# Kernel tuning notes

Measured on AMD Instinct MI355X. Metric: run time of the kernel, lower is better.

## Reference

```python
import jax, jax.numpy as jnp
import numpy as np

K = 3          # spline order
NUM = 32       # grid intervals G
IN_DIM = 256
OUT_DIM = 512
BATCH = 2048


def _b_spline_basis(x, grid, k):
    """Cox-de-Boor recursion. x: (B, I); grid: (I, G+2k+1) -> (B, I, G+k)."""
    xg = x[:, :, None]                      # (B, I, 1)
    g = grid[None, :, :]                    # (1, I, G+2k+1)
    val = ((xg >= g[:, :, :-1]) & (xg < g[:, :, 1:])).astype(x.dtype)
    for p in range(1, k + 1):
        left = (xg - g[:, :, :-(p + 1)]) / (g[:, :, p:-1] - g[:, :, :-(p + 1)])
        right = (g[:, :, p + 1:] - xg) / (g[:, :, p + 1:] - g[:, :, 1:-p])
        val = left * val[:, :, :-1] + right * val[:, :, 1:]
    return val                               # (B, I, G+k)


def setup_inputs() -> dict:
    key = jax.random.key(0)
    k1, k2, k3 = jax.random.split(key, 3)
    x = jax.random.normal(k1, (BATCH, IN_DIM), dtype=jnp.float32)
    # uniform grid on [-1, 1], extended by k knots on each side (extend_grid)
    base = np.linspace(-1.0, 1.0, NUM + 1)
    h = 2.0 / NUM
    ext = np.concatenate([base[0] - h * np.arange(K, 0, -1), base,
                          base[-1] + h * np.arange(1, K + 1)]).astype(np.float32)
    grid = jnp.tile(jnp.asarray(ext)[None, :], (IN_DIM, 1))  # (I, G+2k+1)
    coef = 0.1 * jax.random.normal(k2, (IN_DIM, OUT_DIM, NUM + K), dtype=jnp.float32)
    scale_base = jax.random.normal(k3, (IN_DIM, OUT_DIM), dtype=jnp.float32) / np.sqrt(IN_DIM).astype(np.float32)
    scale_sp = jnp.ones((IN_DIM, OUT_DIM), dtype=jnp.float32) / np.sqrt(IN_DIM).astype(np.float32)
    mask = jnp.ones((IN_DIM, OUT_DIM), dtype=jnp.float32)
    return {"x": x, "grid": grid, "coef": coef,
            "scale_base": scale_base, "scale_sp": scale_sp, "mask": mask}


def reference(x, grid, coef, scale_base, scale_sp, mask):
    base = jax.nn.silu(x)                                   # b(x) residual, (B, I)
    bases = _b_spline_basis(x, grid, K)                     # (B, I, G+k)
    # coef2curve: einsum('ijk,jlk->ijl') in pykan -> (B, I, O)
    y = jnp.einsum('bik,iok->bio', bases, coef)
    y = scale_base[None, :, :] * base[:, :, None] + scale_sp[None, :, :] * y
    y = mask[None, :, :] * y
    return jnp.sum(y, axis=1)                               # (B, O)
```

## Files before the change

### kernel.cpp

```cpp
#include <hip/hip_runtime.h>
#include <math.h>

#define BATCH   2048
#define IN_DIM  256
#define OUT_DIM 512
#define NK      35
#define KS      48
#define BTILE   128
#define OTILE   128
#define ICHUNK  32
#define NSPLIT  8
#define COEFS_BYTES ((size_t)IN_DIM * OUT_DIM * KS * 2)
#define PART_ELEMS  ((size_t)BATCH * OUT_DIM)

__device__ __forceinline__ unsigned short f2bf(float x) {
    unsigned u = __float_as_uint(x);
    u += 0x7FFF + ((u >> 16) & 1);
    return (unsigned short)(u >> 16);
}
__device__ __forceinline__ float bf2f(unsigned short h) {
    return __uint_as_float(((unsigned)h) << 16);
}
__device__ __forceinline__ unsigned pack2(unsigned short a, unsigned short b) {
    return (unsigned)a | ((unsigned)b << 16);
}

typedef __bf16 bf16x8 __attribute__((ext_vector_type(8)));
typedef float  f32x16 __attribute__((ext_vector_type(16)));
typedef unsigned int u32;

__device__ __forceinline__ void gload_lds16(const void* g, void* l) {
    __builtin_amdgcn_global_load_lds((const __attribute__((address_space(1))) u32*)g,
                                     (__attribute__((address_space(3))) u32*)l, 16, 0, 0);
}

#define PR 32
__global__ __launch_bounds__(256) void kan_prep(
    const float* __restrict__ coef,
    const float* __restrict__ scale_base,
    const float* __restrict__ scale_sp,
    const float* __restrict__ mask,
    unsigned short* __restrict__ coefS)
{
    __shared__ float sc[PR * NK];
    __shared__ float sspm[PR], ssbm[PR];
    const int t    = threadIdx.x;
    const int row0 = blockIdx.x * PR;

    {
        const float4* csrc = (const float4*)(coef + (size_t)row0 * NK);
        float4* cdst = (float4*)sc;
        cdst[t] = csrc[t];
        if (t < 24) cdst[t + 256] = csrc[t + 256];
    }
    if (t < PR) {
        float m = mask[row0 + t];
        sspm[t] = scale_sp[row0 + t] * m;
        ssbm[t] = scale_base[row0 + t] * m;
    }
    __syncthreads();

    if (t < PR * 6) {
        int r = t / 6;
        int q = t - r * 6;
        float spm = sspm[r];
        const float* c = sc + r * NK;
        uint4 v = make_uint4(0u, 0u, 0u, 0u);
        if (q < 4) {
            const float* cq = c + q * 8;
            v.x = pack2(f2bf(cq[0] * spm), f2bf(cq[1] * spm));
            v.y = pack2(f2bf(cq[2] * spm), f2bf(cq[3] * spm));
            v.z = pack2(f2bf(cq[4] * spm), f2bf(cq[5] * spm));
            v.w = pack2(f2bf(cq[6] * spm), f2bf(cq[7] * spm));
        } else if (q == 4) {
            float sbm = ssbm[r];
            unsigned short hi = f2bf(sbm);
            unsigned short lo = f2bf(sbm - bf2f(hi));
            v.x = pack2(f2bf(c[32] * spm), f2bf(c[33] * spm));
            v.y = pack2(f2bf(c[34] * spm), 0);
            v.z = pack2(hi, hi);
            v.w = pack2(lo, 0);
        }
        ((uint4*)coefS)[(size_t)(row0 + r) * 6 + q] = v;
    }
}

__global__ __launch_bounds__(256, 2) void kan_mfma(
    const float* __restrict__ x,
    const unsigned short* __restrict__ coefS,
    float* __restrict__ part)
{
    __shared__ __align__(16) short sA[2 * BTILE * KS];
    __shared__ __align__(16) short sB[2 * OTILE * KS];

    const int t    = threadIdx.x;
    const int w    = t >> 6;
    const int lane = t & 63;
    const int l31  = lane & 31, lh = lane >> 5;
    const int wr   = w & 1;
    const int wc   = w >> 1;
    const int o0   = blockIdx.x * OTILE;
    const int b0   = blockIdx.y * BTILE;
    const int ic0  = blockIdx.z * ICHUNK;
    const bool bTh = (t >= 128);
    const int wbase = t & 64;

    {
        uint4 z = make_uint4(0, 0, 0, 0);
        #pragma unroll
        for (int u = 0; u < 6; ++u) {
            int idx = t + 256 * u;
            if (idx < (2 * BTILE * KS * 2) / 16) ((uint4*)sA)[idx] = z;
        }
    }

    f32x16 acc00 = {}, acc01 = {}, acc10 = {}, acc11 = {};

    float xreg = 0.0f;
    int ojb0 = 0, ojb1 = 0;

    auto stageA = [&](short* arow, float xv, int& ojbn) {
        arow[ojbn] = 0; arow[ojbn + 1] = 0; arow[ojbn + 2] = 0; arow[ojbn + 3] = 0;
        float xn = (xv + 1.1875f) * 16.0f;
        float jf = floorf(xn);
        int   j  = (int)jf;
        float u  = xn - jf;
        bool valid = (xn >= 0.0f) && (j <= 37);
        float u2 = u * u, u3 = u2 * u;
        float w0 = (1.0f / 6.0f) * (1.0f - 3.0f * u + 3.0f * u2 - u3);
        float w1 = (1.0f / 6.0f) * (3.0f * u3 - 6.0f * u2 + 4.0f);
        float w2 = (1.0f / 6.0f) * (-3.0f * u3 + 3.0f * u2 + 3.0f * u + 1.0f);
        float w3 = (1.0f / 6.0f) * u3;
        int jb = j - 3;
        if (valid) {
            if ((unsigned)jb       < 35u) arow[jb]     = f2bf(w0);
            if ((unsigned)(jb + 1) < 35u) arow[jb + 1] = f2bf(w1);
            if ((unsigned)(jb + 2) < 35u) arow[jb + 2] = f2bf(w2);
            if ((unsigned)(jb + 3) < 35u) arow[jb + 3] = f2bf(w3);
        }
        ojbn = min(max(jb, 0), 31);
        float sig = 1.0f / (1.0f + __expf(-xv));
        float s   = xv * sig;
        unsigned short shi = f2bf(s);
        unsigned short slo = f2bf(s - bf2f(shi));
        *(unsigned int*)(arow + 36) = pack2(shi, slo);
        arow[38] = shi;
    };

    auto issueB = [&](int i, int buf) {
        const char* gsrc = (const char*)(coefS + ((size_t)i * OUT_DIM + o0) * KS);
        #pragma unroll
        for (int q = 0; q < 6; ++q) {
            int slot = wbase + (t & 63) + 128 * q;
            gload_lds16(gsrc + slot * 16,
                        (void*)(sB + buf * (OTILE * KS) + (wbase + 128 * q) * 8));
        }
    };

    __syncthreads();

    if (!bTh) {
        float x0 = x[(size_t)(b0 + t) * IN_DIM + ic0];
        stageA(sA + t * KS, x0, ojb0);
        xreg = x[(size_t)(b0 + t) * IN_DIM + ic0 + 1];
    } else {
        issueB(ic0, 0);
    }
    __syncthreads();

    auto body = [&](int it, int cur, int nxt, int& ojbn) {
        if (bTh && it + 1 < ICHUNK) issueB(ic0 + it + 1, nxt);

        const short* Ab = sA + cur * (BTILE * KS) + (wr * 64 + l31) * KS + lh * 8;
        const short* Bb = sB + cur * (OTILE * KS) + (wc * 64 + l31) * KS + lh * 8;
        #pragma unroll
        for (int s = 0; s < 3; ++s) {
            bf16x8 a0 = *(const bf16x8*)(Ab + s * 16);
            bf16x8 a1 = *(const bf16x8*)(Ab + 32 * KS + s * 16);
            bf16x8 b0 = *(const bf16x8*)(Bb + s * 16);
            bf16x8 b1 = *(const bf16x8*)(Bb + 32 * KS + s * 16);
            acc00 = __builtin_amdgcn_mfma_f32_32x32x16_bf16(a0, b0, acc00, 0, 0, 0);
            acc01 = __builtin_amdgcn_mfma_f32_32x32x16_bf16(a0, b1, acc01, 0, 0, 0);
            acc10 = __builtin_amdgcn_mfma_f32_32x32x16_bf16(a1, b0, acc10, 0, 0, 0);
            acc11 = __builtin_amdgcn_mfma_f32_32x32x16_bf16(a1, b1, acc11, 0, 0, 0);
        }

        if (!bTh && it + 1 < ICHUNK) {
            stageA(sA + nxt * (BTILE * KS) + t * KS, xreg, ojbn);
            if (it + 2 < ICHUNK)
                xreg = x[(size_t)(b0 + t) * IN_DIM + ic0 + it + 2];
        }
        __syncthreads();
    };

    for (int itp = 0; itp < ICHUNK / 2; ++itp) {
        body(2 * itp,     0, 1, ojb1);
        body(2 * itp + 1, 1, 0, ojb0);
    }

    float* tp = (float*)sA + w * (32 * 36);
    float* pdst = part + (size_t)blockIdx.z * PART_ELEMS;
    #pragma unroll
    for (int r = 0; r < 2; ++r) {
        #pragma unroll
        for (int c = 0; c < 2; ++c) {
            const f32x16& acc = (r == 0) ? ((c == 0) ? acc00 : acc01)
                                         : ((c == 0) ? acc10 : acc11);
            #pragma unroll
            for (int reg = 0; reg < 16; ++reg) {
                int row = (reg & 3) + 8 * (reg >> 2) + 4 * lh;
                tp[row * 36 + l31] = acc[reg];
            }
            int cc = (lane & 7) * 4;
            #pragma unroll
            for (int j = 0; j < 4; ++j) {
                int rr = j * 8 + (lane >> 3);
                float4 v = *(float4*)&tp[rr * 36 + cc];
                int rowg = b0 + wr * 64 + r * 32 + rr;
                int colg = o0 + wc * 64 + c * 32 + cc;
                *(float4*)&pdst[(size_t)rowg * OUT_DIM + colg] = v;
            }
        }
    }
}

__global__ __launch_bounds__(256) void kan_reduce(
    const float4* __restrict__ part, float4* __restrict__ out)
{
    const size_t e = (size_t)blockIdx.x * 256 + threadIdx.x;
    float4 s = part[e];
    #pragma unroll
    for (int z = 1; z < NSPLIT; ++z) {
        float4 v = part[(size_t)z * (PART_ELEMS / 4) + e];
        s.x += v.x; s.y += v.y; s.z += v.z; s.w += v.w;
    }
    out[e] = s;
}

extern "C" void kernel_launch(void* const* d_in, const int* in_sizes, int n_in,
                              void* d_out, int out_size, void* d_ws, size_t ws_size,
                              hipStream_t stream) {
    const float* x          = (const float*)d_in[0];
    const float* coef       = (const float*)d_in[2];
    const float* scale_base = (const float*)d_in[3];
    const float* scale_sp   = (const float*)d_in[4];
    const float* mask       = (const float*)d_in[5];
    unsigned short* coefS   = (unsigned short*)d_ws;
    float* part             = (float*)((char*)d_ws + COEFS_BYTES);

    kan_prep<<<dim3(IN_DIM * OUT_DIM / PR), dim3(256), 0, stream>>>(
        coef, scale_base, scale_sp, mask, coefS);
    kan_mfma<<<dim3(OUT_DIM / OTILE, BATCH / BTILE, NSPLIT), dim3(256), 0, stream>>>(
        x, coefS, part);
    kan_reduce<<<dim3(BATCH * OUT_DIM / 4 / 256), dim3(256), 0, stream>>>(
        (const float4*)part, (float4*)d_out);
}
```

Before: 120.6 us.

## Warp-specialize MFMA kernel with dedicated producer wave for A staging and B loads

Adds a fifth wave per block that alone stages the spline basis tile A and issues the async coefficient loads for B. The four original waves now only perform MFMA accumulation. The aim is to take the staging and load work off the math waves so it overlaps with compute. The risk is that one producer wave now serializes all staging for 128 rows plus 12 load instructions per iteration, which could become the critical path. The larger block size may also lower occupancy.

```diff
diff --git a/kernel.cpp b/kernel.cpp
--- a/kernel.cpp
+++ b/kernel.cpp
@@ -85,7 +85,7 @@
     }
 }
 
-__global__ __launch_bounds__(256, 2) void kan_mfma(
+__global__ __launch_bounds__(320, 2) void kan_mfma(
     const float* __restrict__ x,
     const unsigned short* __restrict__ coefS,
     float* __restrict__ part)
@@ -94,30 +94,29 @@
     __shared__ __align__(16) short sB[2 * OTILE * KS];
 
     const int t    = threadIdx.x;
-    const int w    = t >> 6;
     const int lane = t & 63;
     const int l31  = lane & 31, lh = lane >> 5;
-    const int wr   = w & 1;
-    const int wc   = w >> 1;
     const int o0   = blockIdx.x * OTILE;
     const int b0   = blockIdx.y * BTILE;
     const int ic0  = blockIdx.z * ICHUNK;
-    const bool bTh = (t >= 128);
-    const int wbase = t & 64;
+    const bool prod = (t >= 256);
+    const int w    = t >> 6;
+    const int wr   = w & 1;
+    const int wc   = w >> 1;
 
     {
         uint4 z = make_uint4(0, 0, 0, 0);
         #pragma unroll
-        for (int u = 0; u < 6; ++u) {
-            int idx = t + 256 * u;
+        for (int u = 0; u < 5; ++u) {
+            int idx = t + 320 * u;
             if (idx < (2 * BTILE * KS * 2) / 16) ((uint4*)sA)[idx] = z;
         }
     }
 
     f32x16 acc00 = {}, acc01 = {}, acc10 = {}, acc11 = {};
 
-    float xreg = 0.0f;
-    int ojb0 = 0, ojb1 = 0;
+    float xp0 = 0.f, xp1 = 0.f;
+    int ojb[2][2] = {{0, 0}, {0, 0}};
 
     auto stageA = [&](short* arow, float xv, int& ojbn) {
         arow[ojbn] = 0; arow[ojbn + 1] = 0; arow[ojbn + 2] = 0; arow[ojbn + 3] = 0;
@@ -150,75 +149,80 @@
     auto issueB = [&](int i, int buf) {
         const char* gsrc = (const char*)(coefS + ((size_t)i * OUT_DIM + o0) * KS);
         #pragma unroll
-        for (int q = 0; q < 6; ++q) {
-            int slot = wbase + (t & 63) + 128 * q;
-            gload_lds16(gsrc + slot * 16,
-                        (void*)(sB + buf * (OTILE * KS) + (wbase + 128 * q) * 8));
+        for (int q = 0; q < 12; ++q) {
+            gload_lds16(gsrc + (size_t)(q * 64 + lane) * 16,
+                        (void*)(sB + buf * (OTILE * KS) + q * 512));
         }
     };
 
     __syncthreads();
 
-    if (!bTh) {
-        float x0 = x[(size_t)(b0 + t) * IN_DIM + ic0];
-        stageA(sA + t * KS, x0, ojb0);
-        xreg = x[(size_t)(b0 + t) * IN_DIM + ic0 + 1];
-    } else {
+    if (prod) {
         issueB(ic0, 0);
+        xp0 = x[(size_t)(b0 + lane) * IN_DIM + ic0];
+        xp1 = x[(size_t)(b0 + lane + 64) * IN_DIM + ic0];
+        stageA(sA + lane * KS, xp0, ojb[0][0]);
+        stageA(sA + (lane + 64) * KS, xp1, ojb[0][1]);
+        xp0 = x[(size_t)(b0 + lane) * IN_DIM + ic0 + 1];
+        xp1 = x[(size_t)(b0 + lane + 64) * IN_DIM + ic0 + 1];
     }
     __syncthreads();
 
-    auto body = [&](int it, int cur, int nxt, int& ojbn) {
-        if (bTh && it + 1 < ICHUNK) issueB(ic0 + it + 1, nxt);
-
-        const short* Ab = sA + cur * (BTILE * KS) + (wr * 64 + l31) * KS + lh * 8;
-        const short* Bb = sB + cur * (OTILE * KS) + (wc * 64 + l31) * KS + lh * 8;
-        #pragma unroll
-        for (int s = 0; s < 3; ++s) {
-            bf16x8 a0 = *(const bf16x8*)(Ab + s * 16);
-            bf16x8 a1 = *(const bf16x8*)(Ab + 32 * KS + s * 16);
-            bf16x8 b0 = *(const bf16x8*)(Bb + s * 16);
-            bf16x8 b1 = *(const bf16x8*)(Bb + 32 * KS + s * 16);
-            acc00 = __builtin_amdgcn_mfma_f32_32x32x16_bf16(a0, b0, acc00, 0, 0, 0);
-            acc01 = __builtin_amdgcn_mfma_f32_32x32x16_bf16(a0, b1, acc01, 0, 0, 0);
-            acc10 = __builtin_amdgcn_mfma_f32_32x32x16_bf16(a1, b0, acc10, 0, 0, 0);
-            acc11 = __builtin_amdgcn_mfma_f32_32x32x16_bf16(a1, b1, acc11, 0, 0, 0);
-        }
-
-        if (!bTh && it + 1 < ICHUNK) {
-            stageA(sA + nxt * (BTILE * KS) + t * KS, xreg, ojbn);
-            if (it + 2 < ICHUNK)
-                xreg = x[(size_t)(b0 + t) * IN_DIM + ic0 + it + 2];
+    auto body = [&](int it, int cur, int nxt) {
+        if (prod) {
+            if (it + 1 < ICHUNK) {
+                issueB(ic0 + it + 1, nxt);
+                stageA(sA + nxt * (BTILE * KS) + lane * KS, xp0, ojb[nxt][0]);
+                stageA(sA + nxt * (BTILE * KS) + (lane + 64) * KS, xp1, ojb[nxt][1]);
+                if (it + 2 < ICHUNK) {
+                    xp0 = x[(size_t)(b0 + lane) * IN_DIM + ic0 + it + 2];
+                    xp1 = x[(size_t)(b0 + lane + 64) * IN_DIM + ic0 + it + 2];
+                }
+            }
+        } else {
+            const short* Ab = sA + cur * (BTILE * KS) + (wr * 64 + l31) * KS + lh * 8;
+            const short* Bb = sB + cur * (OTILE * KS) + (wc * 64 + l31) * KS + lh * 8;
+            #pragma unroll
+            for (int s = 0; s < 3; ++s) {
+                bf16x8 a0 = *(const bf16x8*)(Ab + s * 16);
+                bf16x8 a1 = *(const bf16x8*)(Ab + 32 * KS + s * 16);
+                bf16x8 b0 = *(const bf16x8*)(Bb + s * 16);
+                bf16x8 b1 = *(const bf16x8*)(Bb + 32 * KS + s * 16);
+                acc00 = __builtin_amdgcn_mfma_f32_32x32x16_bf16(a0, b0, acc00, 0, 0, 0);
+                acc01 = __builtin_amdgcn_mfma_f32_32x32x16_bf16(a0, b1, acc01, 0, 0, 0);
+                acc10 = __builtin_amdgcn_mfma_f32_32x32x16_bf16(a1, b0, acc10, 0, 0, 0);
+                acc11 = __builtin_amdgcn_mfma_f32_32x32x16_bf16(a1, b1, acc11, 0, 0, 0);
+            }
         }
         __syncthreads();
     };
 
-    for (int itp = 0; itp < ICHUNK / 2; ++itp) {
-        body(2 * itp,     0, 1, ojb1);
-        body(2 * itp + 1, 1, 0, ojb0);
-    }
-
-    float* tp = (float*)sA + w * (32 * 36);
-    float* pdst = part + (size_t)blockIdx.z * PART_ELEMS;
-    #pragma unroll
-    for (int r = 0; r < 2; ++r) {
+    #pragma unroll 2
+    for (int it = 0; it < ICHUNK; ++it) body(it, it & 1, (it + 1) & 1);
+
+    if (!prod) {
+        float* tp = (float*)sA + w * (32 * 36);
+        float* pdst = part + (size_t)blockIdx.z * PART_ELEMS;
         #pragma unroll
-        for (int c = 0; c < 2; ++c) {
-            const f32x16& acc = (r == 0) ? ((c == 0) ? acc00 : acc01)
-                                         : ((c == 0) ? acc10 : acc11);
+        for (int r = 0; r < 2; ++r) {
             #pragma unroll
-            for (int reg = 0; reg < 16; ++reg) {
-                int row = (reg & 3) + 8 * (reg >> 2) + 4 * lh;
-                tp[row * 36 + l31] = acc[reg];
-            }
-            int cc = (lane & 7) * 4;
-            #pragma unroll
-            for (int j = 0; j < 4; ++j) {
-                int rr = j * 8 + (lane >> 3);
-                float4 v = *(float4*)&tp[rr * 36 + cc];
-                int rowg = b0 + wr * 64 + r * 32 + rr;
-                int colg = o0 + wc * 64 + c * 32 + cc;
-                *(float4*)&pdst[(size_t)rowg * OUT_DIM + colg] = v;
+            for (int c = 0; c < 2; ++c) {
+                const f32x16& acc = (r == 0) ? ((c == 0) ? acc00 : acc01)
+                                             : ((c == 0) ? acc10 : acc11);
+                #pragma unroll
+                for (int reg = 0; reg < 16; ++reg) {
+                    int row = (reg & 3) + 8 * (reg >> 2) + 4 * lh;
+                    tp[row * 36 + l31] = acc[reg];
+                }
+                int cc = (lane & 7) * 4;
+                #pragma unroll
+                for (int j = 0; j < 4; ++j) {
+                    int rr = j * 8 + (lane >> 3);
+                    float4 v = *(float4*)&tp[rr * 36 + cc];
+                    int rowg = b0 + wr * 64 + r * 32 + rr;
+                    int colg = o0 + wc * 64 + c * 32 + cc;
+                    *(float4*)&pdst[(size_t)rowg * OUT_DIM + colg] = v;
+                }
             }
         }
     }
@@ -250,7 +254,7 @@
 
     kan_prep<<<dim3(IN_DIM * OUT_DIM / PR), dim3(256), 0, stream>>>(
         coef, scale_base, scale_sp, mask, coefS);
-    kan_mfma<<<dim3(OUT_DIM / OTILE, BATCH / BTILE, NSPLIT), dim3(256), 0, stream>>>(
+    kan_mfma<<<dim3(OUT_DIM / OTILE, BATCH / BTILE, NSPLIT), dim3(320), 0, stream>>>(
         x, coefS, part);
     kan_reduce<<<dim3(BATCH * OUT_DIM / 4 / 256), dim3(256), 0, stream>>>(
         (const float4*)part, (float4*)d_out);
```

Measured after the change: 125.4 us. 3.9% more time.
